# Kernel optimization log

Measured on AMD Instinct MI355X. Metric: run time of the kernel, lower is better.

Reference implementation:

```python
import jax, jax.numpy as jnp
import numpy as np

P_FACTOR = 3.0
EPS = 1e-12  # torch F.normalize eps


def _l2norm(x):
    # F.normalize(x, dim=1): divide by max(||x||_2, eps) along feature dim
    n = jnp.sqrt(jnp.sum(x * x, axis=1, keepdims=True))
    return x / jnp.maximum(n, EPS)


def setup_inputs() -> dict:
    key = jax.random.key(0)
    ks = jax.random.split(key, 7)
    B, N, F, E = 4096, 20000, 768, 512
    X = jax.random.normal(ks[0], (B, F), jnp.float32)
    D = jax.random.normal(ks[1], (N, F), jnp.float32)
    r = jax.random.uniform(ks[2], (N, 1), jnp.float32)  # correctness in [0,1]
    g_w = jax.random.normal(ks[3], (E, F), jnp.float32) * (1.0 / np.sqrt(F))
    g_b = jax.random.normal(ks[4], (E,), jnp.float32) * 0.01
    h_w = jax.random.normal(ks[5], (1, 1), jnp.float32)
    h_b = jax.random.normal(ks[6], (1,), jnp.float32) * 0.01
    return {"X": X, "D": D, "r": r, "g_w": g_w, "g_b": g_b, "h_w": h_w, "h_b": h_b}


def reference(X, D, r, g_w, g_b, h_w, h_b):
    # register_buffer path: r = ex_correct * 2 - 1
    r = r * 2.0 - 1.0
    # g: Linear(feat_dim -> feat_embed_dim) on both queries and exemplars
    Xe = X @ g_w.T + g_b            # [B, E]
    De = D @ g_w.T + g_b            # [N, E]
    # h: Linear(1 -> class_embed_dim)
    rh = r @ h_w.T + h_b            # [N, C]
    # Minerva: cosine similarity -> power-law activation -> weighted retrieval
    a = _l2norm(Xe) @ _l2norm(De).T                 # [B, N]
    a = jnp.sign(a) * jnp.abs(a) ** P_FACTOR        # |s|^p * sign(s)
    logits = a @ rh                                 # [B, C]
    preds = jax.nn.sigmoid(logits)
    return logits, preds
```

## Files before the change

### kernel.cpp

```cpp
#include <hip/hip_runtime.h>
#include <cstdint>


typedef __attribute__((ext_vector_type(4))) float  f32x4;
typedef __attribute__((ext_vector_type(8))) __bf16 bf16x8;
typedef __attribute__((ext_vector_type(4))) __bf16 bf16x4;

constexpr int B = 4096, N = 20000, F = 768, E = 512;

#define AS1CAST(p) ((__attribute__((address_space(1))) unsigned int*)(uintptr_t)(p))
#define AS3CAST(p) ((__attribute__((address_space(3))) unsigned int*)(uintptr_t)(p))

__device__ __forceinline__ void gload_lds16(const void* g, void* l) {
  __builtin_amdgcn_global_load_lds(AS1CAST(g), AS3CAST(l), 16, 0, 0);
}


__global__ void k_prep(const float* __restrict__ X, const float* __restrict__ D,
                       const float* __restrict__ G, const float* __restrict__ r,
                       const float* __restrict__ hw, const float* __restrict__ hb,
                       __bf16* __restrict__ Xb, __bf16* __restrict__ Db,
                       __bf16* __restrict__ Gb, float* __restrict__ rh,
                       float* __restrict__ lg, float* __restrict__ norm2) {
  const int t = blockIdx.x * blockDim.x + threadIdx.x;
  const int stride = gridDim.x * blockDim.x;
  constexpr int nX = B * F / 4, nD = N * F / 4, nG = E * F / 4;
  constexpr int tot = nX + nD + nG;
  for (int i = t; i < tot; i += stride) {
    const float4* src; bf16x4* dst; int off;
    if (i < nX)           { src = (const float4*)X; dst = (bf16x4*)Xb; off = i; }
    else if (i < nX + nD) { src = (const float4*)D; dst = (bf16x4*)Db; off = i - nX; }
    else                  { src = (const float4*)G; dst = (bf16x4*)Gb; off = i - nX - nD; }
    float4 v = src[off];
    bf16x4 o;
    o[0] = (__bf16)v.x; o[1] = (__bf16)v.y; o[2] = (__bf16)v.z; o[3] = (__bf16)v.w;
    dst[off] = o;
  }
  if (t < N) rh[t] = (2.0f * r[t] - 1.0f) * hw[0] + hb[0];
  if (t < B) lg[t] = 0.0f;
  if (t < B + N) norm2[t] = 0.0f;
}


__global__ __launch_bounds__(256, 3)
void k_embed(const __bf16* __restrict__ Xb, const __bf16* __restrict__ Db,
             const __bf16* __restrict__ Gb, const float* __restrict__ bias,
             __bf16* __restrict__ Eb, float* __restrict__ norm2) {
  constexpr int K = F;
  __shared__ __bf16 As[128 * 64];
  __shared__ __bf16 Bs[128 * 64];
  __shared__ float ssum[128];
  const int tid  = threadIdx.x;
  const int wave = tid >> 6;
  const int lane = tid & 63;
  const int by = blockIdx.y;
  const bool isX = (by < B / 128);
  const __bf16* A = isX ? Xb : Db;
  const int m0 = isX ? by * 128 : (by - B / 128) * 128;
  const int Mr = isX ? B : N;
  const int g0 = by * 128;
  const int n0 = blockIdx.x * 128;
  if (tid < 128) ssum[tid] = 0.0f;

  const int srow = tid >> 3;
  const int scg  = (tid & 7) ^ (srow & 7);
  const __bf16* ga[4];
  const __bf16* gb[4];
  __bf16* la[4];
  __bf16* lb[4];
#pragma unroll
  for (int q = 0; q < 4; ++q) {
    const int row = srow + q * 32;
    int arow = m0 + row; if (arow >= Mr) arow = Mr - 1;
    const int brow = n0 + row;
    ga[q] = A  + (size_t)arow * K + scg * 8;
    gb[q] = Gb + (size_t)brow * K + scg * 8;
    la[q] = &As[q * 2048 + tid * 8];
    lb[q] = &Bs[q * 2048 + tid * 8];
  }

  const int mw = (wave & 1) * 64;
  const int nw = (wave >> 1) * 64;
  const int quad = lane >> 4;
  const int l15  = lane & 15;
  f32x4 acc[4][4] = {};

  for (int kb = 0; kb < K; kb += 64) {
#pragma unroll
    for (int q = 0; q < 4; ++q) gload_lds16(ga[q] + kb, la[q]);
#pragma unroll
    for (int q = 0; q < 4; ++q) gload_lds16(gb[q] + kb, lb[q]);
    __syncthreads();
#pragma unroll
    for (int h = 0; h < 2; ++h) {
      bf16x8 af[4], bfr[4];
#pragma unroll
      for (int i = 0; i < 4; ++i) {
        const int rr = mw + i * 16 + l15;
        af[i] = *(const bf16x8*)&As[rr * 64 + ((quad + h * 4) ^ (rr & 7)) * 8];
      }
#pragma unroll
      for (int j = 0; j < 4; ++j) {
        const int rr = nw + j * 16 + l15;
        bfr[j] = *(const bf16x8*)&Bs[rr * 64 + ((quad + h * 4) ^ (rr & 7)) * 8];
      }
#pragma unroll
      for (int i = 0; i < 4; ++i)
#pragma unroll
        for (int j = 0; j < 4; ++j)
          acc[i][j] = __builtin_amdgcn_mfma_f32_16x16x32_bf16(af[i], bfr[j], acc[i][j], 0, 0, 0);
    }
    __syncthreads();
  }

#pragma unroll
  for (int i = 0; i < 4; ++i) {
    float part[4] = {0.0f, 0.0f, 0.0f, 0.0f};
#pragma unroll
    for (int j = 0; j < 4; ++j) {
      const int col = n0 + nw + j * 16 + l15;
      const float bv = bias[col];
#pragma unroll
      for (int rr = 0; rr < 4; ++rr) {
        const int row = mw + i * 16 + quad * 4 + rr;
        if (m0 + row < Mr) {
          const __bf16 hv = (__bf16)(acc[i][j][rr] + bv);
          Eb[(size_t)(g0 + row) * E + col] = hv;
          const float vb = (float)hv;
          part[rr] += vb * vb;
        }
      }
    }
#pragma unroll
    for (int rr = 0; rr < 4; ++rr) {
      float v = part[rr];
      v += __shfl_xor(v, 1);
      v += __shfl_xor(v, 2);
      v += __shfl_xor(v, 4);
      v += __shfl_xor(v, 8);
      if (l15 == 0) atomicAdd(&ssum[mw + i * 16 + quad * 4 + rr], v);
    }
  }
  __syncthreads();
  if (tid < 128 && m0 + tid < Mr) atomicAdd(&norm2[g0 + tid], ssum[tid]);
}


__global__ __launch_bounds__(256, 3)
void k_minerva(const __bf16* __restrict__ Xe, const __bf16* __restrict__ De,
               const float* __restrict__ norm2, const float* __restrict__ rh,
               float* __restrict__ logits) {
  constexpr int K  = 512;
  constexpr int MT = B / 128;
  constexpr int NT = (N + 127) / 128;
  constexpr int W  = 20;
  __shared__ __bf16 As[128 * 64];
  __shared__ __bf16 Bs[128 * 64];
  __shared__ float lsum[128];
  const int tid  = threadIdx.x;
  const int lane = tid & 63;
  const int wave = tid >> 6;

  const int bid   = blockIdx.x;
  const int panel = bid / (W * MT);
  const int bn    = panel * W;
  const int rem   = bid - panel * (W * MT);
  const int mt    = rem % MT;
  const int nt    = bn + rem / MT;
  const int m0 = mt * 128, n0 = nt * 128;
  if (tid < 128) lsum[tid] = 0.0f;

  const int srow = tid >> 3;
  const int scg  = (tid & 7) ^ (srow & 7);
  const __bf16* ga[4];
  const __bf16* gb[4];
  __bf16* la[4];
  __bf16* lb[4];
#pragma unroll
  for (int q = 0; q < 4; ++q) {
    const int row = srow + q * 32;
    const int arow = m0 + row;
    int brow = n0 + row; if (brow >= N) brow = N - 1;
    ga[q] = Xe + (size_t)arow * K + scg * 8;
    gb[q] = De + (size_t)brow * K + scg * 8;
    la[q] = &As[q * 2048 + tid * 8];
    lb[q] = &Bs[q * 2048 + tid * 8];
  }

  const int mw = (wave & 1) * 64;
  const int nw = (wave >> 1) * 64;
  const int quad = lane >> 4;
  const int l15  = lane & 15;
  f32x4 acc[4][4] = {};

  for (int kb = 0; kb < K; kb += 64) {
#pragma unroll
    for (int q = 0; q < 4; ++q) gload_lds16(ga[q] + kb, la[q]);
#pragma unroll
    for (int q = 0; q < 4; ++q) gload_lds16(gb[q] + kb, lb[q]);
    __syncthreads();
#pragma unroll
    for (int h = 0; h < 2; ++h) {
      bf16x8 af[4], bfr[4];
#pragma unroll
      for (int i = 0; i < 4; ++i) {
        const int rr = mw + i * 16 + l15;
        af[i] = *(const bf16x8*)&As[rr * 64 + ((quad + h * 4) ^ (rr & 7)) * 8];
      }
#pragma unroll
      for (int j = 0; j < 4; ++j) {
        const int rr = nw + j * 16 + l15;
        bfr[j] = *(const bf16x8*)&Bs[rr * 64 + ((quad + h * 4) ^ (rr & 7)) * 8];
      }
#pragma unroll
      for (int i = 0; i < 4; ++i)
#pragma unroll
        for (int j = 0; j < 4; ++j)
          acc[i][j] = __builtin_amdgcn_mfma_f32_16x16x32_bf16(af[i], bfr[j], acc[i][j], 0, 0, 0);
    }
    __syncthreads();
  }

  float id3rh[4];
#pragma unroll
  for (int j = 0; j < 4; ++j) {
    const int col = n0 + nw + j * 16 + l15;
    if (col < N) {
      const float id = 1.0f / fmaxf(sqrtf(norm2[B + col]), 1e-12f);
      id3rh[j] = id * id * id * rh[col];
    } else id3rh[j] = 0.0f;
  }
#pragma unroll
  for (int i = 0; i < 4; ++i) {
    float ix3[4];
#pragma unroll
    for (int rr = 0; rr < 4; ++rr) {
      const int row = m0 + mw + i * 16 + quad * 4 + rr;
      const float ix = 1.0f / fmaxf(sqrtf(norm2[row]), 1e-12f);
      ix3[rr] = ix * ix * ix;
    }
    float part[4] = {0.0f, 0.0f, 0.0f, 0.0f};
#pragma unroll
    for (int j = 0; j < 4; ++j)
#pragma unroll
      for (int rr = 0; rr < 4; ++rr) {
        const float a = acc[i][j][rr];
        const float a2 = a * a;
        part[rr] = fmaf(a2 * a, id3rh[j], part[rr]);
      }
#pragma unroll
    for (int rr = 0; rr < 4; ++rr) {
      float v = part[rr] * ix3[rr];
      v += __shfl_xor(v, 1);
      v += __shfl_xor(v, 2);
      v += __shfl_xor(v, 4);
      v += __shfl_xor(v, 8);
      if (l15 == 0) atomicAdd(&lsum[mw + i * 16 + quad * 4 + rr], v);
    }
  }
  __syncthreads();
  if (tid < 128) atomicAdd(&logits[m0 + tid], lsum[tid]);
}


__global__ void k_finalize(const float* __restrict__ logits, float* __restrict__ out, int n) {
  int i = blockIdx.x * blockDim.x + threadIdx.x;
  if (i < n) {
    float L = logits[i];
    out[i] = L;
    out[n + i] = 1.0f / (1.0f + expf(-L));
  }
}


extern "C" void kernel_launch(void* const* d_in, const int* in_sizes, int n_in,
                              void* d_out, int out_size, void* d_ws, size_t ws_size,
                              hipStream_t stream) {
  const float* X   = (const float*)d_in[0];
  const float* D   = (const float*)d_in[1];
  const float* r   = (const float*)d_in[2];
  const float* g_w = (const float*)d_in[3];
  const float* g_b = (const float*)d_in[4];
  const float* h_w = (const float*)d_in[5];
  const float* h_b = (const float*)d_in[6];
  float* out = (float*)d_out;

  char* ws = (char*)d_ws;
  __bf16* Xb    = (__bf16*)(ws + 0);
  __bf16* Db    = (__bf16*)(ws + 6291456);
  __bf16* Gb    = (__bf16*)(ws + 37011456);
  __bf16* Eb    = (__bf16*)(ws + 37797888);
  float*  rh    = (float*) (ws + 62472192);
  float*  norm2 = (float*) (ws + 62552192);
  float*  lg    = (float*) (ws + 62648576);

  k_prep<<<2048, 256, 0, stream>>>(X, D, g_w, r, h_w, h_b, Xb, Db, Gb, rh, lg, norm2);

  k_embed<<<dim3(E / 128, B / 128 + (N + 127) / 128), 256, 0, stream>>>(
      Xb, Db, Gb, g_b, Eb, norm2);

  k_minerva<<<157 * 32, 256, 0, stream>>>(Eb, Eb + (size_t)B * E, norm2, rh, lg);

  k_finalize<<<(B + 255) / 256, 256, 0, stream>>>(lg, out, B);
}
```

Measured before the change: 257.5 us.

## Fuse bf16 conversion into embed GEMM and finalize into minerva via last-block counter

```diff
diff --git a/kernel.cpp b/kernel.cpp
--- a/kernel.cpp
+++ b/kernel.cpp
@@ -4,9 +4,10 @@
 
 typedef __attribute__((ext_vector_type(4))) float  f32x4;
 typedef __attribute__((ext_vector_type(8))) __bf16 bf16x8;
-typedef __attribute__((ext_vector_type(4))) __bf16 bf16x4;
 
 constexpr int B = 4096, N = 20000, F = 768, E = 512;
+constexpr int NROWS = 24576;
+constexpr unsigned MINERVA_BLOCKS = 32u * 160u;
 
 #define AS1CAST(p) ((__attribute__((address_space(1))) unsigned int*)(uintptr_t)(p))
 #define AS3CAST(p) ((__attribute__((address_space(3))) unsigned int*)(uintptr_t)(p))
@@ -15,68 +16,48 @@
   __builtin_amdgcn_global_load_lds(AS1CAST(g), AS3CAST(l), 16, 0, 0);
 }
 
-
-__global__ void k_prep(const float* __restrict__ X, const float* __restrict__ D,
-                       const float* __restrict__ G, const float* __restrict__ r,
-                       const float* __restrict__ hw, const float* __restrict__ hb,
-                       __bf16* __restrict__ Xb, __bf16* __restrict__ Db,
-                       __bf16* __restrict__ Gb, float* __restrict__ rh,
-                       float* __restrict__ lg, float* __restrict__ norm2) {
-  const int t = blockIdx.x * blockDim.x + threadIdx.x;
-  const int stride = gridDim.x * blockDim.x;
-  constexpr int nX = B * F / 4, nD = N * F / 4, nG = E * F / 4;
-  constexpr int tot = nX + nD + nG;
-  for (int i = t; i < tot; i += stride) {
-    const float4* src; bf16x4* dst; int off;
-    if (i < nX)           { src = (const float4*)X; dst = (bf16x4*)Xb; off = i; }
-    else if (i < nX + nD) { src = (const float4*)D; dst = (bf16x4*)Db; off = i - nX; }
-    else                  { src = (const float4*)G; dst = (bf16x4*)Gb; off = i - nX - nD; }
-    float4 v = src[off];
-    bf16x4 o;
-    o[0] = (__bf16)v.x; o[1] = (__bf16)v.y; o[2] = (__bf16)v.z; o[3] = (__bf16)v.w;
-    dst[off] = o;
-  }
-  if (t < N) rh[t] = (2.0f * r[t] - 1.0f) * hw[0] + hb[0];
-  if (t < B) lg[t] = 0.0f;
-  if (t < B + N) norm2[t] = 0.0f;
-}
+__device__ unsigned g_done = 0;
 
 
 __global__ __launch_bounds__(256, 3)
-void k_embed(const __bf16* __restrict__ Xb, const __bf16* __restrict__ Db,
-             const __bf16* __restrict__ Gb, const float* __restrict__ bias,
-             __bf16* __restrict__ Eb, float* __restrict__ norm2) {
-  constexpr int K = F;
+void k_embed(const float* __restrict__ X, const float* __restrict__ D,
+             const float* __restrict__ G, const float* __restrict__ bias,
+             __bf16* __restrict__ Eb, float* __restrict__ norm2p,
+             float* __restrict__ lg) {
   __shared__ __bf16 As[128 * 64];
   __shared__ __bf16 Bs[128 * 64];
-  __shared__ float ssum[128];
+  __shared__ float lsum[128];
   const int tid  = threadIdx.x;
+  const int bid  = blockIdx.x;
   const int wave = tid >> 6;
   const int lane = tid & 63;
-  const int by = blockIdx.y;
-  const bool isX = (by < B / 128);
-  const __bf16* A = isX ? Xb : Db;
-  const int m0 = isX ? by * 128 : (by - B / 128) * 128;
+
+  if (bid == 0) {
+    for (int i = tid; i < B; i += 256) lg[i] = 0.0f;
+  }
+
+  const int bx = bid / 192;
+  const int by = bid % 192;
+  const bool isX = (by < 32);
+  const float* A = isX ? X : D;
+  const int m0 = isX ? by * 128 : (by - 32) * 128;
   const int Mr = isX ? B : N;
   const int g0 = by * 128;
-  const int n0 = blockIdx.x * 128;
-  if (tid < 128) ssum[tid] = 0.0f;
-
-  const int srow = tid >> 3;
-  const int scg  = (tid & 7) ^ (srow & 7);
-  const __bf16* ga[4];
-  const __bf16* gb[4];
-  __bf16* la[4];
-  __bf16* lb[4];
+  const int n0 = bx * 128;
+  if (tid < 128) lsum[tid] = 0.0f;
+
+  const int cg    = tid & 7;
+  const int rbase = tid >> 3;
+  const int sw    = ((cg ^ (rbase & 7)) * 8);
+  size_t aoff[4], boff[4];
+  int    lidx[4];
 #pragma unroll
   for (int q = 0; q < 4; ++q) {
-    const int row = srow + q * 32;
-    int arow = m0 + row; if (arow >= Mr) arow = Mr - 1;
-    const int brow = n0 + row;
-    ga[q] = A  + (size_t)arow * K + scg * 8;
-    gb[q] = Gb + (size_t)brow * K + scg * 8;
-    la[q] = &As[q * 2048 + tid * 8];
-    lb[q] = &Bs[q * 2048 + tid * 8];
+    const int rt = rbase + 32 * q;
+    int arow = m0 + rt; if (arow >= Mr) arow = Mr - 1;
+    aoff[q] = (size_t)arow * F + cg * 8;
+    boff[q] = (size_t)(n0 + rt) * F + cg * 8;
+    lidx[q] = rt * 64 + sw;
   }
 
   const int mw = (wave & 1) * 64;
@@ -85,11 +66,25 @@
   const int l15  = lane & 15;
   f32x4 acc[4][4] = {};
 
-  for (int kb = 0; kb < K; kb += 64) {
-#pragma unroll
-    for (int q = 0; q < 4; ++q) gload_lds16(ga[q] + kb, la[q]);
-#pragma unroll
-    for (int q = 0; q < 4; ++q) gload_lds16(gb[q] + kb, lb[q]);
+  for (int kb = 0; kb < F; kb += 64) {
+#pragma unroll
+    for (int q = 0; q < 4; ++q) {
+      const float4 v0 = *(const float4*)(A + aoff[q] + kb);
+      const float4 v1 = *(const float4*)(A + aoff[q] + kb + 4);
+      bf16x8 t;
+      t[0] = (__bf16)v0.x; t[1] = (__bf16)v0.y; t[2] = (__bf16)v0.z; t[3] = (__bf16)v0.w;
+      t[4] = (__bf16)v1.x; t[5] = (__bf16)v1.y; t[6] = (__bf16)v1.z; t[7] = (__bf16)v1.w;
+      *(bf16x8*)&As[lidx[q]] = t;
+    }
+#pragma unroll
+    for (int q = 0; q < 4; ++q) {
+      const float4 v0 = *(const float4*)(G + boff[q] + kb);
+      const float4 v1 = *(const float4*)(G + boff[q] + kb + 4);
+      bf16x8 t;
+      t[0] = (__bf16)v0.x; t[1] = (__bf16)v0.y; t[2] = (__bf16)v0.z; t[3] = (__bf16)v0.w;
+      t[4] = (__bf16)v1.x; t[5] = (__bf16)v1.y; t[6] = (__bf16)v1.z; t[7] = (__bf16)v1.w;
+      *(bf16x8*)&Bs[lidx[q]] = t;
+    }
     __syncthreads();
 #pragma unroll
     for (int h = 0; h < 2; ++h) {
@@ -138,137 +133,146 @@
       v += __shfl_xor(v, 2);
       v += __shfl_xor(v, 4);
       v += __shfl_xor(v, 8);
-      if (l15 == 0) atomicAdd(&ssum[mw + i * 16 + quad * 4 + rr], v);
+      if (l15 == 0) atomicAdd(&lsum[mw + i * 16 + quad * 4 + rr], v);
     }
   }
   __syncthreads();
-  if (tid < 128 && m0 + tid < Mr) atomicAdd(&norm2[g0 + tid], ssum[tid]);
+  if (tid < 128) norm2p[(size_t)bx * NROWS + g0 + tid] = lsum[tid];
 }
 
 
 __global__ __launch_bounds__(256, 3)
-void k_minerva(const __bf16* __restrict__ Xe, const __bf16* __restrict__ De,
-               const float* __restrict__ norm2, const float* __restrict__ rh,
-               float* __restrict__ logits) {
-  constexpr int K  = 512;
-  constexpr int MT = B / 128;
-  constexpr int NT = (N + 127) / 128;
-  constexpr int W  = 20;
+void k_minerva(const __bf16* __restrict__ Eb, const float* __restrict__ norm2p,
+               const float* __restrict__ r, const float* __restrict__ hw,
+               const float* __restrict__ hb, float* __restrict__ lg,
+               float* __restrict__ out) {
   __shared__ __bf16 As[128 * 64];
   __shared__ __bf16 Bs[128 * 64];
   __shared__ float lsum[128];
+  __shared__ int amLast;
   const int tid  = threadIdx.x;
+  const int bid  = blockIdx.x;
+  const int wave = tid >> 6;
   const int lane = tid & 63;
-  const int wave = tid >> 6;
-
-  const int bid   = blockIdx.x;
-  const int panel = bid / (W * MT);
-  const int bn    = panel * W;
-  const int rem   = bid - panel * (W * MT);
-  const int mt    = rem % MT;
-  const int nt    = bn + rem / MT;
-  const int m0 = mt * 128, n0 = nt * 128;
-  if (tid < 128) lsum[tid] = 0.0f;
-
-  const int srow = tid >> 3;
-  const int scg  = (tid & 7) ^ (srow & 7);
-  const __bf16* ga[4];
-  const __bf16* gb[4];
-  __bf16* la[4];
-  __bf16* lb[4];
-#pragma unroll
-  for (int q = 0; q < 4; ++q) {
-    const int row = srow + q * 32;
-    const int arow = m0 + row;
-    int brow = n0 + row; if (brow >= N) brow = N - 1;
-    ga[q] = Xe + (size_t)arow * K + scg * 8;
-    gb[q] = De + (size_t)brow * K + scg * 8;
-    la[q] = &As[q * 2048 + tid * 8];
-    lb[q] = &Bs[q * 2048 + tid * 8];
-  }
-
-  const int mw = (wave & 1) * 64;
-  const int nw = (wave >> 1) * 64;
-  const int quad = lane >> 4;
-  const int l15  = lane & 15;
-  f32x4 acc[4][4] = {};
-
-  for (int kb = 0; kb < K; kb += 64) {
-#pragma unroll
-    for (int q = 0; q < 4; ++q) gload_lds16(ga[q] + kb, la[q]);
-#pragma unroll
-    for (int q = 0; q < 4; ++q) gload_lds16(gb[q] + kb, lb[q]);
+  const int mt = bid / 160;
+  const int nt = bid % 160;
+
+  if (nt < 157) {
+    const int m0 = mt * 128, n0 = nt * 128;
+    if (tid < 128) lsum[tid] = 0.0f;
+    const __bf16* Xe = Eb;
+    const __bf16* De = Eb + (size_t)B * E;
+
+    const int srow = tid >> 3;
+    const int scg  = (tid & 7) ^ (srow & 7);
+    const __bf16* ga[4]; const __bf16* gb[4]; int li[4];
+#pragma unroll
+    for (int q = 0; q < 4; ++q) {
+      const int row = srow + 32 * q;
+      const int arow = m0 + row;
+      int brow = n0 + row; if (brow >= N) brow = N - 1;
+      ga[q] = Xe + (size_t)arow * E + scg * 8;
+      gb[q] = De + (size_t)brow * E + scg * 8;
+      li[q] = q * 2048 + tid * 8;
+    }
+
+    const int mw = (wave & 1) * 64;
+    const int nw = (wave >> 1) * 64;
+    const int quad = lane >> 4;
+    const int l15  = lane & 15;
+    f32x4 acc[4][4] = {};
+
+    for (int kb = 0; kb < E; kb += 64) {
+#pragma unroll
+      for (int q = 0; q < 4; ++q) gload_lds16(ga[q] + kb, &As[li[q]]);
+#pragma unroll
+      for (int q = 0; q < 4; ++q) gload_lds16(gb[q] + kb, &Bs[li[q]]);
+      __syncthreads();
+#pragma unroll
+      for (int h = 0; h < 2; ++h) {
+        bf16x8 af[4], bfr[4];
+#pragma unroll
+        for (int i = 0; i < 4; ++i) {
+          const int rr = mw + i * 16 + l15;
+          af[i] = *(const bf16x8*)&As[rr * 64 + ((quad + h * 4) ^ (rr & 7)) * 8];
+        }
+#pragma unroll
+        for (int j = 0; j < 4; ++j) {
+          const int rr = nw + j * 16 + l15;
+          bfr[j] = *(const bf16x8*)&Bs[rr * 64 + ((quad + h * 4) ^ (rr & 7)) * 8];
+        }
+#pragma unroll
+        for (int i = 0; i < 4; ++i)
+#pragma unroll
+          for (int j = 0; j < 4; ++j)
+            acc[i][j] = __builtin_amdgcn_mfma_f32_16x16x32_bf16(af[i], bfr[j], acc[i][j], 0, 0, 0);
+      }
+      __syncthreads();
+    }
+
+    const float hwv = hw[0], hbv = hb[0];
+    float id3rh[4];
+#pragma unroll
+    for (int j = 0; j < 4; ++j) {
+      const int col = n0 + nw + j * 16 + l15;
+      if (col < N) {
+        const int gr = B + col;
+        const float nd2 = norm2p[gr] + norm2p[NROWS + gr]
+                        + norm2p[2 * NROWS + gr] + norm2p[3 * NROWS + gr];
+        const float id = 1.0f / fmaxf(sqrtf(nd2), 1e-12f);
+        const float rhv = (2.0f * r[col] - 1.0f) * hwv + hbv;
+        id3rh[j] = id * id * id * rhv;
+      } else id3rh[j] = 0.0f;
+    }
+#pragma unroll
+    for (int i = 0; i < 4; ++i) {
+      float ix3[4];
+#pragma unroll
+      for (int rr = 0; rr < 4; ++rr) {
+        const int row = m0 + mw + i * 16 + quad * 4 + rr;
+        const float nx2 = norm2p[row] + norm2p[NROWS + row]
+                        + norm2p[2 * NROWS + row] + norm2p[3 * NROWS + row];
+        const float ix = 1.0f / fmaxf(sqrtf(nx2), 1e-12f);
+        ix3[rr] = ix * ix * ix;
+      }
+      float part[4] = {0.0f, 0.0f, 0.0f, 0.0f};
+#pragma unroll
+      for (int j = 0; j < 4; ++j)
+#pragma unroll
+        for (int rr = 0; rr < 4; ++rr) {
+          const float a = acc[i][j][rr];
+          part[rr] = fmaf(a * a * a, id3rh[j], part[rr]);
+        }
+#pragma unroll
+      for (int rr = 0; rr < 4; ++rr) {
+        float v = part[rr] * ix3[rr];
+        v += __shfl_xor(v, 1);
+        v += __shfl_xor(v, 2);
+        v += __shfl_xor(v, 4);
+        v += __shfl_xor(v, 8);
+        if (l15 == 0) atomicAdd(&lsum[mw + i * 16 + quad * 4 + rr], v);
+      }
+    }
     __syncthreads();
-#pragma unroll
-    for (int h = 0; h < 2; ++h) {
-      bf16x8 af[4], bfr[4];
-#pragma unroll
-      for (int i = 0; i < 4; ++i) {
-        const int rr = mw + i * 16 + l15;
-        af[i] = *(const bf16x8*)&As[rr * 64 + ((quad + h * 4) ^ (rr & 7)) * 8];
-      }
-#pragma unroll
-      for (int j = 0; j < 4; ++j) {
-        const int rr = nw + j * 16 + l15;
-        bfr[j] = *(const bf16x8*)&Bs[rr * 64 + ((quad + h * 4) ^ (rr & 7)) * 8];
-      }
-#pragma unroll
-      for (int i = 0; i < 4; ++i)
-#pragma unroll
-        for (int j = 0; j < 4; ++j)
-          acc[i][j] = __builtin_amdgcn_mfma_f32_16x16x32_bf16(af[i], bfr[j], acc[i][j], 0, 0, 0);
-    }
-    __syncthreads();
-  }
-
-  float id3rh[4];
-#pragma unroll
-  for (int j = 0; j < 4; ++j) {
-    const int col = n0 + nw + j * 16 + l15;
-    if (col < N) {
-      const float id = 1.0f / fmaxf(sqrtf(norm2[B + col]), 1e-12f);
-      id3rh[j] = id * id * id * rh[col];
-    } else id3rh[j] = 0.0f;
-  }
-#pragma unroll
-  for (int i = 0; i < 4; ++i) {
-    float ix3[4];
-#pragma unroll
-    for (int rr = 0; rr < 4; ++rr) {
-      const int row = m0 + mw + i * 16 + quad * 4 + rr;
-      const float ix = 1.0f / fmaxf(sqrtf(norm2[row]), 1e-12f);
-      ix3[rr] = ix * ix * ix;
-    }
-    float part[4] = {0.0f, 0.0f, 0.0f, 0.0f};
-#pragma unroll
-    for (int j = 0; j < 4; ++j)
-#pragma unroll
-      for (int rr = 0; rr < 4; ++rr) {
-        const float a = acc[i][j][rr];
-        const float a2 = a * a;
-        part[rr] = fmaf(a2 * a, id3rh[j], part[rr]);
-      }
-#pragma unroll
-    for (int rr = 0; rr < 4; ++rr) {
-      float v = part[rr] * ix3[rr];
-      v += __shfl_xor(v, 1);
-      v += __shfl_xor(v, 2);
-      v += __shfl_xor(v, 4);
-      v += __shfl_xor(v, 8);
-      if (l15 == 0) atomicAdd(&lsum[mw + i * 16 + quad * 4 + rr], v);
-    }
-  }
+    if (tid < 128) atomicAdd(&lg[m0 + tid], lsum[tid]);
+  }
+
   __syncthreads();
-  if (tid < 128) atomicAdd(&logits[m0 + tid], lsum[tid]);
-}
-
-
-__global__ void k_finalize(const float* __restrict__ logits, float* __restrict__ out, int n) {
-  int i = blockIdx.x * blockDim.x + threadIdx.x;
-  if (i < n) {
-    float L = logits[i];
-    out[i] = L;
-    out[n + i] = 1.0f / (1.0f + expf(-L));
+  if (tid == 0) {
+    __builtin_amdgcn_fence(__ATOMIC_RELEASE, "agent");
+    const unsigned prev =
+        __hip_atomic_fetch_add(&g_done, 1u, __ATOMIC_ACQ_REL, __HIP_MEMORY_SCOPE_AGENT);
+    amLast = (prev == MINERVA_BLOCKS - 1u);
+    if (amLast)
+      __hip_atomic_store(&g_done, 0u, __ATOMIC_RELAXED, __HIP_MEMORY_SCOPE_AGENT);
+  }
+  __syncthreads();
+  if (amLast) {
+    for (int i = tid; i < B; i += 256) {
+      const float L = __hip_atomic_load(&lg[i], __ATOMIC_RELAXED, __HIP_MEMORY_SCOPE_AGENT);
+      out[i] = L;
+      out[B + i] = 1.0f / (1.0f + expf(-L));
+    }
   }
 }
 
@@ -286,20 +290,11 @@
   float* out = (float*)d_out;
 
   char* ws = (char*)d_ws;
-  __bf16* Xb    = (__bf16*)(ws + 0);
-  __bf16* Db    = (__bf16*)(ws + 6291456);
-  __bf16* Gb    = (__bf16*)(ws + 37011456);
-  __bf16* Eb    = (__bf16*)(ws + 37797888);
-  float*  rh    = (float*) (ws + 62472192);
-  float*  norm2 = (float*) (ws + 62552192);
-  float*  lg    = (float*) (ws + 62648576);
-
-  k_prep<<<2048, 256, 0, stream>>>(X, D, g_w, r, h_w, h_b, Xb, Db, Gb, rh, lg, norm2);
-
-  k_embed<<<dim3(E / 128, B / 128 + (N + 127) / 128), 256, 0, stream>>>(
-      Xb, Db, Gb, g_b, Eb, norm2);
-
-  k_minerva<<<157 * 32, 256, 0, stream>>>(Eb, Eb + (size_t)B * E, norm2, rh, lg);
-
-  k_finalize<<<(B + 255) / 256, 256, 0, stream>>>(lg, out, B);
+  __bf16* Eb     = (__bf16*)(ws + 0);
+  float*  norm2p = (float*) (ws + 24674304);
+  float*  lg     = (float*) (ws + 25067520);
+
+  k_embed<<<4 * 192, 256, 0, stream>>>(X, D, g_w, g_b, Eb, norm2p, lg);
+
+  k_minerva<<<MINERVA_BLOCKS, 256, 0, stream>>>(Eb, norm2p, r, h_w, h_b, lg, out);
 }
```

Result: slower. 363.5 us (+41.1%).
